# Optimization experiments

Hardware: AMD Instinct MI355X
Metric: run time of the kernel (lower is better)

The kernel has to match this reference:

```python
import jax, jax.numpy as jnp
import numpy as np
import math

B, T, D, H = 4, 2048, 1024, 16
ND = D // H  # head dim = 64


def setup_inputs() -> dict:
    key = jax.random.key(0)
    ks = jax.random.split(key, 12)
    s = 1.0 / math.sqrt(D)
    inp = {
        "q": jax.random.normal(ks[0], (B, T, D), jnp.float32),
        "k": jax.random.normal(ks[1], (B, T, D), jnp.float32),
        "v": jax.random.normal(ks[2], (B, T, D), jnp.float32),
        # nn.Linear params: weight [out,in], bias [out]
        "wq": jax.random.normal(ks[3], (D, D), jnp.float32) * s,
        "bq": jax.random.normal(ks[4], (D,), jnp.float32) * s,
        "wk": jax.random.normal(ks[5], (D, D), jnp.float32) * s,
        "bk": jax.random.normal(ks[6], (D,), jnp.float32) * s,
        "wv": jax.random.normal(ks[7], (D, D), jnp.float32) * s,
        "bv": jax.random.normal(ks[8], (D,), jnp.float32) * s,
        "wo": jax.random.normal(ks[9], (D, D), jnp.float32) * s,
        "bo": jax.random.normal(ks[10], (D,), jnp.float32) * s,
        # causal mask: 1 where attending allowed, 0 -> -inf
        "mask": jnp.tril(jnp.ones((T, T), jnp.int32)),
    }
    return inp


def reference(q, k, v, wq, bq, wk, bk, wv, bv, wo, bo, mask):
    batch, time, dim = q.shape
    n_d = dim // H
    # NOTE: original module (faithfully reproduced bug) computes k and v from q
    Q = q @ wq.T + bq
    K = q @ wk.T + bk
    V = q @ wv.T + bv
    # [B, T, D] -> [B, H, T, nd]
    Q = Q.reshape(batch, time, H, n_d).transpose(0, 2, 1, 3)
    K = K.reshape(batch, time, H, n_d).transpose(0, 2, 1, 3)
    V = V.reshape(batch, time, H, n_d).transpose(0, 2, 1, 3)
    score = jnp.einsum("bhqd,bhkd->bhqk", Q, K) / math.sqrt(n_d)
    score = jnp.where(mask == 0, -jnp.inf, score)
    # original uses nn.Softmax(dim=-2): normalize over the QUERY axis
    attn = jax.nn.softmax(score, axis=-2)
    out = jnp.einsum("bhqk,bhkd->bhqd", attn, V)
    out = out.transpose(0, 2, 1, 3).reshape(batch, time, dim)
    return out @ wo.T + bo
```

## Files before the change

### kernel.cpp

```cpp
#include <hip/hip_runtime.h>
#include <stdint.h>

#define B_  4
#define T_  2048
#define D_  1024
#define H_  16
#define ND_ 64
#define M_  (B_ * T_)

typedef unsigned short u16;
typedef __bf16 bf8  __attribute__((ext_vector_type(8)));
typedef float  f4   __attribute__((ext_vector_type(4)));
typedef u16    u16x8 __attribute__((ext_vector_type(8)));

__device__ inline u16 f2bf(float f) {
    unsigned int x = __builtin_bit_cast(unsigned int, f);
    x += 0x7fffu + ((x >> 16) & 1u);
    return (u16)(x >> 16);
}
__device__ inline unsigned int cvt_pk_bf16(float a, float b) {
    unsigned int r;
    asm("v_cvt_pk_bf16_f32 %0, %1, %2" : "=v"(r) : "v"(a), "v"(b));
    return r;
}
__device__ inline f4 mfma16(bf8 a, bf8 b, f4 c) {
    return __builtin_amdgcn_mfma_f32_16x16x32_bf16(a, b, c, 0, 0, 0);
}
__device__ inline void async16(const void* g, void* l) {
    auto gp = reinterpret_cast<const __attribute__((address_space(1))) unsigned int*>(
        reinterpret_cast<uintptr_t>(g));
    auto lp = reinterpret_cast<__attribute__((address_space(3))) unsigned int*>(
        reinterpret_cast<uintptr_t>(l));
    __builtin_amdgcn_global_load_lds(gp, lp, 16, 0, 0);
}

__global__ __launch_bounds__(256)
void cvt_bf16(const float* __restrict__ in, u16* __restrict__ out, int n) {
    int i = (blockIdx.x * blockDim.x + threadIdx.x) * 8;
    if (i + 8 <= n) {
        float4 a = *(const float4*)(in + i);
        float4 b = *(const float4*)(in + i + 4);
        u16x8 o;
        o[0] = f2bf(a.x); o[1] = f2bf(a.y); o[2] = f2bf(a.z); o[3] = f2bf(a.w);
        o[4] = f2bf(b.x); o[5] = f2bf(b.y); o[6] = f2bf(b.z); o[7] = f2bf(b.w);
        *(u16x8*)(out + i) = o;
    }
}

__global__ __launch_bounds__(256)
void cvt_w4(const float* __restrict__ w0, const float* __restrict__ w1,
            const float* __restrict__ w2, const float* __restrict__ w3,
            u16* __restrict__ o0, u16* __restrict__ o1,
            u16* __restrict__ o2, u16* __restrict__ o3) {
    const float* in; u16* out;
    switch (blockIdx.y) {
        case 0:  in = w0; out = o0; break;
        case 1:  in = w1; out = o1; break;
        case 2:  in = w2; out = o2; break;
        default: in = w3; out = o3; break;
    }
    int i = (blockIdx.x * blockDim.x + threadIdx.x) * 8;
    float4 a = *(const float4*)(in + i);
    float4 b = *(const float4*)(in + i + 4);
    u16x8 o;
    o[0] = f2bf(a.x); o[1] = f2bf(a.y); o[2] = f2bf(a.z); o[3] = f2bf(a.w);
    o[4] = f2bf(b.x); o[5] = f2bf(b.y); o[6] = f2bf(b.z); o[7] = f2bf(b.w);
    *(u16x8*)(out + i) = o;
}

__global__ __launch_bounds__(256, 2)
void gemm_qkv(const u16* __restrict__ A, const u16* __restrict__ W,
              const float* __restrict__ bq, const float* __restrict__ bk,
              const float* __restrict__ bvp,
              u16* __restrict__ Qh, u16* __restrict__ Kh, u16* __restrict__ Vtr) {
    constexpr int K = 1024;
    __shared__ __attribute__((aligned(16))) u16 sA[128 * 32];
    __shared__ __attribute__((aligned(16))) u16 sB[128 * 32];
    const int tid  = threadIdx.x;
    const int wave = tid >> 6;
    const int lane = tid & 63;
    const int m0 = blockIdx.y * 128;
    const int n0 = blockIdx.x * 128;
    const int wm = (wave & 1) * 64;
    const int wn = (wave >> 1) * 64;

    f4 acc[4][4] = {};

    const int srow = wave * 32 + (lane >> 2);
    const int scol = (lane & 3) * 8;
    const u16* gA = A + (size_t)(m0 + srow) * K + scol;
    const u16* gB = W + (size_t)(n0 + srow) * K + scol;
    u16* lA0 = sA + (wave * 32) * 32;
    u16* lA1 = sA + (wave * 32 + 16) * 32;
    u16* lB0 = sB + (wave * 32) * 32;
    u16* lB1 = sB + (wave * 32 + 16) * 32;

    const int row = lane & 15;
    const int qo  = (lane >> 4) * 8;

    for (int k0 = 0; k0 < K; k0 += 32) {
        async16(gA + k0, lA0);
        async16(gA + k0 + (size_t)16 * K, lA1);
        async16(gB + k0, lB0);
        async16(gB + k0 + (size_t)16 * K, lB1);
        __syncthreads();

        bf8 af[4], bfr[4];
#pragma unroll
        for (int i = 0; i < 4; i++)
            af[i] = *(const bf8*)(sA + (wm + i * 16 + row) * 32 + qo);
#pragma unroll
        for (int i = 0; i < 4; i++)
            bfr[i] = *(const bf8*)(sB + (wn + i * 16 + row) * 32 + qo);
#pragma unroll
        for (int mi = 0; mi < 4; mi++)
#pragma unroll
            for (int ni = 0; ni < 4; ni++)
                acc[mi][ni] = mfma16(af[mi], bfr[ni], acc[mi][ni]);
        __syncthreads();
    }

    const int which = n0 >> 10;
    const float* bias = which == 0 ? bq : (which == 1 ? bk : bvp);
    u16* outQK = which == 0 ? Qh : Kh;

#pragma unroll
    for (int ni = 0; ni < 4; ni++) {
        const int n  = n0 + wn + ni * 16 + row;
        const int nl = n & 1023;
        const float bvv = bias[nl];
#pragma unroll
        for (int mi = 0; mi < 4; mi++) {
#pragma unroll
            for (int r = 0; r < 4; r++) {
                const int m = m0 + wm + mi * 16 + (lane >> 4) * 4 + r;
                float v = acc[mi][ni][r] + bvv;
                if (which == 0) v *= 0.125f;
                if (which < 2) {
                    size_t idx = (((size_t)((m >> 11) * H_ + (nl >> 6)) * T_) + (m & (T_ - 1))) * ND_ +
                                 (nl & (ND_ - 1));
                    outQK[idx] = f2bf(v);
                } else {
                    size_t idx = ((size_t)(((m >> 11) * H_ + (nl >> 6)) * ND_ + (nl & (ND_ - 1)))) * T_ +
                                 (m & (T_ - 1));
                    Vtr[idx] = f2bf(v);
                }
            }
        }
    }
}

__global__ __launch_bounds__(256, 2)
void gemm_out(const u16* __restrict__ A, const u16* __restrict__ W,
              const float* __restrict__ bias, float* __restrict__ Cout) {
    constexpr int K = 1024;
    constexpr int N = 1024;
    __shared__ __attribute__((aligned(16))) u16 sA[128 * 32];
    __shared__ __attribute__((aligned(16))) u16 sB[128 * 32];
    const int tid  = threadIdx.x;
    const int wave = tid >> 6;
    const int lane = tid & 63;
    const int m0 = blockIdx.y * 128;
    const int n0 = blockIdx.x * 128;
    const int wm = (wave & 1) * 64;
    const int wn = (wave >> 1) * 64;

    f4 acc[4][4] = {};

    const int srow = wave * 32 + (lane >> 2);
    const int scol = (lane & 3) * 8;
    const u16* gA = A + (size_t)(m0 + srow) * K + scol;
    const u16* gB = W + (size_t)(n0 + srow) * K + scol;
    u16* lA0 = sA + (wave * 32) * 32;
    u16* lA1 = sA + (wave * 32 + 16) * 32;
    u16* lB0 = sB + (wave * 32) * 32;
    u16* lB1 = sB + (wave * 32 + 16) * 32;

    const int row = lane & 15;
    const int qo  = (lane >> 4) * 8;

    for (int k0 = 0; k0 < K; k0 += 32) {
        async16(gA + k0, lA0);
        async16(gA + k0 + (size_t)16 * K, lA1);
        async16(gB + k0, lB0);
        async16(gB + k0 + (size_t)16 * K, lB1);
        __syncthreads();

        bf8 af[4], bfr[4];
#pragma unroll
        for (int i = 0; i < 4; i++)
            af[i] = *(const bf8*)(sA + (wm + i * 16 + row) * 32 + qo);
#pragma unroll
        for (int i = 0; i < 4; i++)
            bfr[i] = *(const bf8*)(sB + (wn + i * 16 + row) * 32 + qo);
#pragma unroll
        for (int mi = 0; mi < 4; mi++)
#pragma unroll
            for (int ni = 0; ni < 4; ni++)
                acc[mi][ni] = mfma16(af[mi], bfr[ni], acc[mi][ni]);
        __syncthreads();
    }

#pragma unroll
    for (int ni = 0; ni < 4; ni++) {
        const int n = n0 + wn + ni * 16 + row;
        const float bv = bias[n];
#pragma unroll
        for (int mi = 0; mi < 4; mi++) {
#pragma unroll
            for (int r = 0; r < 4; r++) {
                const int m = m0 + wm + mi * 16 + (lane >> 4) * 4 + r;
                Cout[(size_t)m * N + n] = acc[mi][ni][r] + bv;
            }
        }
    }
}

__global__ __launch_bounds__(256)
void col_sum(const u16* __restrict__ Qh, const u16* __restrict__ Kh,
             float* __restrict__ Ic) {
    __shared__ __attribute__((aligned(16))) u16 sQ[2][32 * 72];
    const int bh   = blockIdx.y;
    const int tid  = threadIdx.x;
    const int wave = tid >> 6;
    const int lane = tid & 63;
    const int l15  = lane & 15;
    const int quad = lane >> 4;
    const int qo   = quad * 8;
    const int sr   = tid >> 3;
    const int sc   = (tid & 7) * 8;
    const u16* Qb = Qh + (size_t)bh * T_ * ND_;
    const u16* Kb = Kh + (size_t)bh * T_ * ND_;

#pragma unroll
    for (int half = 0; half < 2; half++) {
        const int strip = half ? (15 - (int)blockIdx.x) : (int)blockIdx.x;
        const int c0  = strip * 128;
        const int c0w = c0 + wave * 32;
        bf8 b0[2], b1[2];
#pragma unroll
        for (int g = 0; g < 2; g++) {
            b0[g] = *(const bf8*)(Kb + (size_t)(c0w + g * 16 + l15) * ND_ + qo);
            b1[g] = *(const bf8*)(Kb + (size_t)(c0w + g * 16 + l15) * ND_ + 32 + qo);
        }
        float acc[2][4] = {};
        int p = 0;
        u16x8 pq = *(const u16x8*)(Qb + (size_t)(c0 + sr) * ND_ + sc);
        for (int qt = c0; qt < T_; qt += 32) {
            *(u16x8*)(&sQ[p][sr * 72 + sc]) = pq;
            __syncthreads();
            if (qt + 32 < T_)
                pq = *(const u16x8*)(Qb + (size_t)(qt + 32 + sr) * ND_ + sc);
            const bool masked = qt < c0 + 128;
#pragma unroll
            for (int sub = 0; sub < 2; sub++) {
                const int rho = sub * 16 + l15;
                bf8 a0 = *(const bf8*)(&sQ[p][rho * 72 + qo]);
                bf8 a1 = *(const bf8*)(&sQ[p][rho * 72 + 32 + qo]);
#pragma unroll
                for (int g = 0; g < 2; g++) {
                    f4 s = {0.f, 0.f, 0.f, 0.f};
                    s = mfma16(a0, b0[g], s);
                    s = mfma16(a1, b1[g], s);
                    if (masked) {
#pragma unroll
                        for (int r = 0; r < 4; r++) {
                            const int qg = qt + sub * 16 + quad * 4 + r;
                            const int cg = c0w + g * 16 + l15;
                            acc[g][r] += (qg >= cg) ? __expf(s[r]) : 0.f;
                        }
                    } else {
#pragma unroll
                        for (int r = 0; r < 4; r++)
                            acc[g][r] += __expf(s[r]);
                    }
                }
            }
            p ^= 1;
        }
        __syncthreads();
#pragma unroll
        for (int g = 0; g < 2; g++) {
            float l = acc[g][0] + acc[g][1] + acc[g][2] + acc[g][3];
            l += __shfl_xor(l, 16);
            l += __shfl_xor(l, 32);
            if (lane < 16) Ic[(size_t)bh * T_ + c0w + g * 16 + l15] = 1.f / l;
        }
    }
}

__global__ __launch_bounds__(256, 2)
void attn_out(const u16* __restrict__ Qh, const u16* __restrict__ Kh,
              const u16* __restrict__ Vt, const float* __restrict__ Ic,
              u16* __restrict__ AO) {
    __shared__ __attribute__((aligned(16))) u16 sK[64 * 72];
    __shared__ __attribute__((aligned(16))) u16 sVt[64 * 72];
    __shared__ __attribute__((aligned(16))) u16 sP[4][32 * 64];
    const int bh   = blockIdx.x;
    const int b    = bh >> 4;
    const int h    = bh & 15;
    const int tid  = threadIdx.x;
    const int wave = tid >> 6;
    const int lane = tid & 63;
    const int l15  = lane & 15;
    const int quad = lane >> 4;
    const int qo   = quad * 8;
    const int swz  = (l15 & 7) << 4;

    const u16* Qb = Qh + (size_t)bh * T_ * ND_;
    const u16* Kb = Kh + (size_t)bh * T_ * ND_;
    const u16* Vb = Vt + (size_t)bh * ND_ * T_;
    const float* ic = Ic + (size_t)bh * T_;

    const int sr = tid >> 3;
    const int sc = (tid & 7) * 8;
    char* pw = (char*)sP[wave];

#pragma unroll
    for (int half = 0; half < 2; half++) {
        const int jj = half ? (15 - (int)blockIdx.y) : (int)blockIdx.y;
        const int qb = jj * 128;
        const int kend = qb + 128;

        const int qw = qb + wave * 32;
        bf8 aq[2][2];
#pragma unroll
        for (int qs = 0; qs < 2; qs++)
#pragma unroll
            for (int dh = 0; dh < 2; dh++)
                aq[qs][dh] = *(const bf8*)(Qb + (size_t)(qw + qs * 16 + l15) * ND_ + dh * 32 + qo);

        f4 o[2][4] = {};

        u16x8 pk0 = *(const u16x8*)(Kb + (size_t)sr * ND_ + sc);
        u16x8 pk1 = *(const u16x8*)(Kb + (size_t)(sr + 32) * ND_ + sc);
        u16x8 pv0 = *(const u16x8*)(Vb + (size_t)sr * T_ + sc);
        u16x8 pv1 = *(const u16x8*)(Vb + (size_t)(sr + 32) * T_ + sc);

        for (int kt = 0; kt < kend; kt += 64) {
            *(u16x8*)(sK + sr * 72 + sc) = pk0;
            *(u16x8*)(sK + (sr + 32) * 72 + sc) = pk1;
            *(u16x8*)(sVt + sr * 72 + sc) = pv0;
            *(u16x8*)(sVt + (sr + 32) * 72 + sc) = pv1;
            __syncthreads();

            const int ktn = kt + 64;
            if (ktn < kend) {
                pk0 = *(const u16x8*)(Kb + (size_t)(ktn + sr) * ND_ + sc);
                pk1 = *(const u16x8*)(Kb + (size_t)(ktn + sr + 32) * ND_ + sc);
                pv0 = *(const u16x8*)(Vb + (size_t)sr * T_ + ktn + sc);
                pv1 = *(const u16x8*)(Vb + (size_t)(sr + 32) * T_ + ktn + sc);
            }

#pragma unroll
            for (int ks = 0; ks < 4; ks++) {
                bf8 kb0 = *(const bf8*)(sK + (ks * 16 + l15) * 72 + qo);
                bf8 kb1 = *(const bf8*)(sK + (ks * 16 + l15) * 72 + 32 + qo);
                const f4 icv = *(const f4*)(ic + kt + ks * 16 + quad * 4);
                const int kbase = kt + ks * 16 + quad * 4;
#pragma unroll
                for (int qs = 0; qs < 2; qs++) {
                    f4 s = {0.f, 0.f, 0.f, 0.f};
                    s = mfma16(kb0, aq[qs][0], s);
                    s = mfma16(kb1, aq[qs][1], s);
                    f4 p;
                    if (kt + ks * 16 + 15 <= qw + qs * 16) {
#pragma unroll
                        for (int r = 0; r < 4; r++) p[r] = __expf(s[r]) * icv[r];
                    } else {
                        const int qg = qw + qs * 16 + l15;
#pragma unroll
                        for (int r = 0; r < 4; r++)
                            p[r] = (kbase + r <= qg) ? __expf(s[r]) * icv[r] : 0.f;
                    }
                    uint2 w;
                    w.x = cvt_pk_bf16(p[0], p[1]);
                    w.y = cvt_pk_bf16(p[2], p[3]);
                    *(uint2*)(pw + (((qs * 16 + l15) * 128 + ks * 32 + quad * 8) ^ swz)) = w;
                }
            }
#pragma unroll
            for (int st = 0; st < 2; st++) {
                bf8 ap0 = *(const bf8*)(pw + ((l15 * 128 + st * 64 + quad * 16) ^ swz));
                bf8 ap1 = *(const bf8*)(pw + (((16 + l15) * 128 + st * 64 + quad * 16) ^ swz));
#pragma unroll
                for (int ds = 0; ds < 4; ds++) {
                    bf8 bv = *(const bf8*)(sVt + (ds * 16 + l15) * 72 + st * 32 + qo);
                    o[0][ds] = mfma16(ap0, bv, o[0][ds]);
                    o[1][ds] = mfma16(ap1, bv, o[1][ds]);
                }
            }
            __syncthreads();
        }

#pragma unroll
        for (int qs = 0; qs < 2; qs++)
#pragma unroll
            for (int ds = 0; ds < 4; ds++)
#pragma unroll
                for (int r = 0; r < 4; r++) {
                    const int q = qw + qs * 16 + quad * 4 + r;
                    const int d = ds * 16 + l15;
                    AO[((size_t)(b * T_ + q)) * D_ + h * ND_ + d] = f2bf(o[qs][ds][r]);
                }
    }
}

extern "C" void kernel_launch(void* const* d_in, const int* in_sizes, int n_in,
                              void* d_out, int out_size, void* d_ws, size_t ws_size,
                              hipStream_t stream) {
    (void)in_sizes; (void)n_in; (void)out_size; (void)ws_size;
    const float* q  = (const float*)d_in[0];
    const float* wq = (const float*)d_in[3];
    const float* bq = (const float*)d_in[4];
    const float* wk = (const float*)d_in[5];
    const float* bk = (const float*)d_in[6];
    const float* wv = (const float*)d_in[7];
    const float* bv = (const float*)d_in[8];
    const float* wo = (const float*)d_in[9];
    const float* bo = (const float*)d_in[10];

    const size_t SZ = (size_t)M_ * D_;
    const size_t WSZ = (size_t)D_ * D_;
    u16* Qh  = (u16*)d_ws;
    u16* Kh  = Qh + SZ;
    u16* Vtr = Kh + SZ;
    u16* qbf = Vtr + SZ;
    u16* AO  = qbf;
    u16* wqb = qbf + SZ;
    u16* wkb = wqb + WSZ;
    u16* wvb = wkb + WSZ;
    u16* wob = wvb + WSZ;
    float* Ic = (float*)(wob + WSZ);

    cvt_bf16<<<dim3(SZ / 8 / 256), 256, 0, stream>>>(q, qbf, (int)SZ);
    cvt_w4<<<dim3(WSZ / 8 / 256, 4), 256, 0, stream>>>(wq, wk, wv, wo,
                                                       wqb, wkb, wvb, wob);

    dim3 gqkv(3 * D_ / 128, M_ / 128);
    gemm_qkv<<<gqkv, 256, 0, stream>>>(qbf, wqb, bq, bk, bv, Qh, Kh, Vtr);

    dim3 gcs(8, B_ * H_);
    col_sum<<<gcs, 256, 0, stream>>>(Qh, Kh, Ic);

    dim3 ga(B_ * H_, 8);
    attn_out<<<ga, 256, 0, stream>>>(Qh, Kh, Vtr, Ic, AO);

    dim3 gp(D_ / 128, M_ / 128);
    gemm_out<<<gp, 256, 0, stream>>>(AO, wob, bo, (float*)d_out);
}
```

Measured before the change: 383.4 us.

## Double-buffer LDS tiles in QKV and output GEMMs to overlap loads with MFMA

```diff
diff --git a/kernel.cpp b/kernel.cpp
--- a/kernel.cpp
+++ b/kernel.cpp
@@ -74,8 +74,8 @@
               const float* __restrict__ bvp,
               u16* __restrict__ Qh, u16* __restrict__ Kh, u16* __restrict__ Vtr) {
     constexpr int K = 1024;
-    __shared__ __attribute__((aligned(16))) u16 sA[128 * 32];
-    __shared__ __attribute__((aligned(16))) u16 sB[128 * 32];
+    __shared__ __attribute__((aligned(16))) u16 sA[2][128 * 32];
+    __shared__ __attribute__((aligned(16))) u16 sB[2][128 * 32];
     const int tid  = threadIdx.x;
     const int wave = tid >> 6;
     const int lane = tid & 63;
@@ -90,34 +90,41 @@
     const int scol = (lane & 3) * 8;
     const u16* gA = A + (size_t)(m0 + srow) * K + scol;
     const u16* gB = W + (size_t)(n0 + srow) * K + scol;
-    u16* lA0 = sA + (wave * 32) * 32;
-    u16* lA1 = sA + (wave * 32 + 16) * 32;
-    u16* lB0 = sB + (wave * 32) * 32;
-    u16* lB1 = sB + (wave * 32 + 16) * 32;
+    const int lo0 = (wave * 32) * 32;
+    const int lo1 = (wave * 32 + 16) * 32;
 
     const int row = lane & 15;
     const int qo  = (lane >> 4) * 8;
 
+    async16(gA, sA[0] + lo0);
+    async16(gA + (size_t)16 * K, sA[0] + lo1);
+    async16(gB, sB[0] + lo0);
+    async16(gB + (size_t)16 * K, sB[0] + lo1);
+    __syncthreads();
+
+    int p = 0;
     for (int k0 = 0; k0 < K; k0 += 32) {
-        async16(gA + k0, lA0);
-        async16(gA + k0 + (size_t)16 * K, lA1);
-        async16(gB + k0, lB0);
-        async16(gB + k0 + (size_t)16 * K, lB1);
-        __syncthreads();
-
+        const int kn = k0 + 32;
+        if (kn < K) {
+            async16(gA + kn, sA[p ^ 1] + lo0);
+            async16(gA + kn + (size_t)16 * K, sA[p ^ 1] + lo1);
+            async16(gB + kn, sB[p ^ 1] + lo0);
+            async16(gB + kn + (size_t)16 * K, sB[p ^ 1] + lo1);
+        }
         bf8 af[4], bfr[4];
 #pragma unroll
         for (int i = 0; i < 4; i++)
-            af[i] = *(const bf8*)(sA + (wm + i * 16 + row) * 32 + qo);
+            af[i] = *(const bf8*)(sA[p] + (wm + i * 16 + row) * 32 + qo);
 #pragma unroll
         for (int i = 0; i < 4; i++)
-            bfr[i] = *(const bf8*)(sB + (wn + i * 16 + row) * 32 + qo);
+            bfr[i] = *(const bf8*)(sB[p] + (wn + i * 16 + row) * 32 + qo);
 #pragma unroll
         for (int mi = 0; mi < 4; mi++)
 #pragma unroll
             for (int ni = 0; ni < 4; ni++)
                 acc[mi][ni] = mfma16(af[mi], bfr[ni], acc[mi][ni]);
         __syncthreads();
+        p ^= 1;
     }
 
     const int which = n0 >> 10;
@@ -155,8 +162,8 @@
               const float* __restrict__ bias, float* __restrict__ Cout) {
     constexpr int K = 1024;
     constexpr int N = 1024;
-    __shared__ __attribute__((aligned(16))) u16 sA[128 * 32];
-    __shared__ __attribute__((aligned(16))) u16 sB[128 * 32];
+    __shared__ __attribute__((aligned(16))) u16 sA[2][128 * 32];
+    __shared__ __attribute__((aligned(16))) u16 sB[2][128 * 32];
     const int tid  = threadIdx.x;
     const int wave = tid >> 6;
     const int lane = tid & 63;
@@ -171,34 +178,41 @@
     const int scol = (lane & 3) * 8;
     const u16* gA = A + (size_t)(m0 + srow) * K + scol;
     const u16* gB = W + (size_t)(n0 + srow) * K + scol;
-    u16* lA0 = sA + (wave * 32) * 32;
-    u16* lA1 = sA + (wave * 32 + 16) * 32;
-    u16* lB0 = sB + (wave * 32) * 32;
-    u16* lB1 = sB + (wave * 32 + 16) * 32;
+    const int lo0 = (wave * 32) * 32;
+    const int lo1 = (wave * 32 + 16) * 32;
 
     const int row = lane & 15;
     const int qo  = (lane >> 4) * 8;
 
+    async16(gA, sA[0] + lo0);
+    async16(gA + (size_t)16 * K, sA[0] + lo1);
+    async16(gB, sB[0] + lo0);
+    async16(gB + (size_t)16 * K, sB[0] + lo1);
+    __syncthreads();
+
+    int p = 0;
     for (int k0 = 0; k0 < K; k0 += 32) {
-        async16(gA + k0, lA0);
-        async16(gA + k0 + (size_t)16 * K, lA1);
-        async16(gB + k0, lB0);
-        async16(gB + k0 + (size_t)16 * K, lB1);
-        __syncthreads();
-
+        const int kn = k0 + 32;
+        if (kn < K) {
+            async16(gA + kn, sA[p ^ 1] + lo0);
+            async16(gA + kn + (size_t)16 * K, sA[p ^ 1] + lo1);
+            async16(gB + kn, sB[p ^ 1] + lo0);
+            async16(gB + kn + (size_t)16 * K, sB[p ^ 1] + lo1);
+        }
         bf8 af[4], bfr[4];
 #pragma unroll
         for (int i = 0; i < 4; i++)
-            af[i] = *(const bf8*)(sA + (wm + i * 16 + row) * 32 + qo);
+            af[i] = *(const bf8*)(sA[p] + (wm + i * 16 + row) * 32 + qo);
 #pragma unroll
         for (int i = 0; i < 4; i++)
-            bfr[i] = *(const bf8*)(sB + (wn + i * 16 + row) * 32 + qo);
+            bfr[i] = *(const bf8*)(sB[p] + (wn + i * 16 + row) * 32 + qo);
 #pragma unroll
         for (int mi = 0; mi < 4; mi++)
 #pragma unroll
             for (int ni = 0; ni < 4; ni++)
                 acc[mi][ni] = mfma16(af[mi], bfr[ni], acc[mi][ni]);
         __syncthreads();
+        p ^= 1;
     }
 
 #pragma unroll
```

New measurement: 382.8 us. About the same (-0.2%).
